# Kernel optimization log

Measured on AMD Instinct MI355X. Metric: run time of the kernel, lower is better.

The kernel has to match this reference:

```python
import jax, jax.numpy as jnp
import numpy as np

GRID = 10
C_IN = 4          # input_dim // (grid*grid) = 400 // 100
HID = 128         # lstm hidden_dim
NV = 6            # num_vehicles
PH = 10           # pred_horizon
BN_EPS = 1e-5


def setup_inputs() -> dict:
    key = jax.random.key(0)
    ks = jax.random.split(key, 20)
    def n(k, shape, scale=0.05):
        return jax.random.normal(k, shape, jnp.float32) * scale
    return {
        "observations": jax.random.normal(ks[0], (1024, 32, 400), jnp.float32),
        # CNN
        "conv1_w": n(ks[1], (16, C_IN, 3, 3)), "conv1_b": n(ks[2], (16,)),
        "conv2_w": n(ks[3], (32, 16, 3, 3)), "conv2_b": n(ks[4], (32,)),
        # FCN (BatchNorm in eval mode: running stats + affine)
        "fc1_w": n(ks[5], (128, 128)), "fc1_b": n(ks[6], (128,)),
        "bn1_gamma": jnp.ones((128,), jnp.float32), "bn1_beta": jnp.zeros((128,), jnp.float32),
        "bn1_mean": jnp.zeros((128,), jnp.float32), "bn1_var": jnp.ones((128,), jnp.float32),
        "fc2_w": n(ks[7], (64, 128)), "fc2_b": n(ks[8], (64,)),
        "bn2_gamma": jnp.ones((64,), jnp.float32), "bn2_beta": jnp.zeros((64,), jnp.float32),
        "bn2_mean": jnp.zeros((64,), jnp.float32), "bn2_var": jnp.ones((64,), jnp.float32),
        # encoder LSTM (torch gate order i,f,g,o; b = b_ih + b_hh fused)
        "enc_w_ih": n(ks[9], (4 * HID, 64)), "enc_w_hh": n(ks[10], (4 * HID, HID)),
        "enc_b": n(ks[11], (4 * HID,)),
        # decoder LSTM
        "dec_w_ih": n(ks[12], (4 * HID, HID)), "dec_w_hh": n(ks[13], (4 * HID, HID)),
        "dec_b": n(ks[14], (4 * HID,)),
        # output head
        "out_w": n(ks[15], (2 * NV, HID)), "out_b": n(ks[16], (2 * NV,)),
    }


def _conv(x, w, b):
    y = jax.lax.conv_general_dilated(x, w, (1, 1), "SAME",
                                     dimension_numbers=("NCHW", "OIHW", "NCHW"))
    return y + b[None, :, None, None]


def _maxpool2(x):
    # MaxPool2d(2,2) with floor (drops odd trailing row/col) == VALID
    return jax.lax.reduce_window(x, -jnp.inf, jax.lax.max, (1, 1, 2, 2), (1, 1, 2, 2), "VALID")


def _bn(x, g, b, m, v):
    return (x - m) * jax.lax.rsqrt(v + BN_EPS) * g + b


def _lstm_cell(x, h, c, w_ih, w_hh, b):
    gates = x @ w_ih.T + h @ w_hh.T + b
    i, f, g, o = jnp.split(gates, 4, axis=-1)
    c_new = jax.nn.sigmoid(f) * c + jax.nn.sigmoid(i) * jnp.tanh(g)
    h_new = jax.nn.sigmoid(o) * jnp.tanh(c_new)
    return h_new, c_new


def reference(observations, conv1_w, conv1_b, conv2_w, conv2_b,
              fc1_w, fc1_b, bn1_gamma, bn1_beta, bn1_mean, bn1_var,
              fc2_w, fc2_b, bn2_gamma, bn2_beta, bn2_mean, bn2_var,
              enc_w_ih, enc_w_hh, enc_b, dec_w_ih, dec_w_hh, dec_b,
              out_w, out_b):
    B, T, D = observations.shape
    # ---- fuse the per-frame Python loop: batch all B*T frames at once ----
    x = observations.reshape(B * T, C_IN, GRID, GRID)
    x = _maxpool2(jax.nn.relu(_conv(x, conv1_w, conv1_b)))   # [BT,16,5,5]
    x = _maxpool2(jax.nn.relu(_conv(x, conv2_w, conv2_b)))   # [BT,32,2,2]
    x = x.reshape(B * T, -1)                                 # [BT,128]
    x = jax.nn.relu(_bn(x @ fc1_w.T + fc1_b, bn1_gamma, bn1_beta, bn1_mean, bn1_var))
    x = jax.nn.relu(_bn(x @ fc2_w.T + fc2_b, bn2_gamma, bn2_beta, bn2_mean, bn2_var))
    feats = x.reshape(B, T, 64)

    # ---- encoder LSTM ----
    h0 = jnp.zeros((B, HID), feats.dtype)
    c0 = jnp.zeros((B, HID), feats.dtype)
    def enc_step(carry, xt):
        h, c = carry
        h, c = _lstm_cell(xt, h, c, enc_w_ih, enc_w_hh, enc_b)
        return (h, c), h
    (h_n, c_n), hs = jax.lax.scan(enc_step, (h0, c0), jnp.swapaxes(feats, 0, 1))
    dec_x = hs[-1]  # encoder_output[:, -1]

    def dec_step(carry, _):
        x_in, h, c = carry
        h, c = _lstm_cell(x_in, h, c, dec_w_ih, dec_w_hh, dec_b)
        pred = h @ out_w.T + out_b
        return (h, h, c), pred
    _, preds = jax.lax.scan(dec_step, (dec_x, h_n, c_n), None, length=PH)
    return jnp.swapaxes(preds, 0, 1)  # [B, PH, 2*NV]
```

## Files before the change

kernel.cpp:

```cpp
#include <hip/hip_runtime.h>
#include <hip/hip_bf16.h>
#include <hip/hip_fp16.h>

constexpr int GT = 32768;
constexpr int TSEQ = 32;

typedef _Float16 h2 __attribute__((ext_vector_type(2)));

#if defined(__has_builtin)
#if __has_builtin(__builtin_amdgcn_fdot2)
#define FDOT2(a, b, c) __builtin_amdgcn_fdot2((a), (b), (c), false)
#endif
#endif
#ifndef FDOT2
#define FDOT2(a, b, c) fmaf((float)(a).x, (float)(b).x, fmaf((float)(a).y, (float)(b).y, (c)))
#endif

__device__ __forceinline__ h2 pack2(float a, float b) {
  h2 v; v.x = (_Float16)a; v.y = (_Float16)b; return v;
}

constexpr size_t OBS_T  = 0;
constexpr size_t POOL1H = 13107200;
constexpr size_t POOL2H = 0;
constexpr size_t Y1H    = 2097152;
constexpr size_t FEATSH = 19660800;
constexpr size_t GX     = 0;
constexpr size_t WB     = 26214400;
constexpr size_t W_C1   = WB + 0;
constexpr size_t W_C2H  = WB + 576;
constexpr size_t W_F1H  = WB + 2880;
constexpr size_t B_F1   = WB + 11072;
constexpr size_t W_F2H  = WB + 11200;
constexpr size_t B_F2   = WB + 15296;
constexpr size_t W_ENCXH= WB + 15360;
constexpr size_t W_ENCHH= WB + 31744;
constexpr size_t B_ENC  = WB + 64512;
constexpr size_t W_DECH = WB + 65024;
constexpr size_t B_DEC  = WB + 97792;

__device__ __forceinline__ float sigf(float x)  { return 1.f / (1.f + __expf(-x)); }
__device__ __forceinline__ float tanhfast(float x) { return 1.f - 2.f / (__expf(2.f * x) + 1.f); }

__global__ __launch_bounds__(256) void k_setup(
    const float* __restrict__ c1w, const float* __restrict__ c2w,
    const float* __restrict__ f1w, const float* __restrict__ f1b,
    const float* __restrict__ g1, const float* __restrict__ be1,
    const float* __restrict__ m1, const float* __restrict__ v1,
    const float* __restrict__ f2w, const float* __restrict__ f2b,
    const float* __restrict__ g2, const float* __restrict__ be2,
    const float* __restrict__ m2, const float* __restrict__ v2,
    const float* __restrict__ ewih, const float* __restrict__ ewhh, const float* __restrict__ eb,
    const float* __restrict__ dwih, const float* __restrict__ dwhh, const float* __restrict__ db,
    float* __restrict__ ws) {
  h2* wsh = (h2*)ws;
  long i = (long)blockIdx.x * 256 + threadIdx.x;
  if (i < 576)  { int c = i & 15, r = i >> 4; ws[W_C1 + i] = c1w[c * 36 + r]; return; }
  i -= 576;
  if (i < 2304) { int co = i & 31, q = i >> 5; int ci2 = q / 9, t9 = q % 9;
    wsh[W_C2H + i] = pack2(c2w[co * 144 + (2 * ci2) * 9 + t9],
                           c2w[co * 144 + (2 * ci2 + 1) * 9 + t9]); return; }
  i -= 2304;
  if (i < 8192) { int j = i & 127, q = i >> 7; int co2 = q >> 2, pos = q & 3;
    float s = g1[j] * rsqrtf(v1[j] + 1e-5f);
    wsh[W_F1H + i] = pack2(f1w[j * 128 + 8 * co2 + pos] * s,
                           f1w[j * 128 + 8 * co2 + 4 + pos] * s); return; }
  i -= 8192;
  if (i < 128) { int j = i; float s = g1[j] * rsqrtf(v1[j] + 1e-5f);
    ws[B_F1 + i] = (f1b[j] - m1[j]) * s + be1[j]; return; }
  i -= 128;
  if (i < 4096) { int j = i & 63, k2 = i >> 6;
    float s = g2[j] * rsqrtf(v2[j] + 1e-5f);
    wsh[W_F2H + i] = pack2(f2w[j * 128 + 2 * k2] * s,
                           f2w[j * 128 + 2 * k2 + 1] * s); return; }
  i -= 4096;
  if (i < 64) { int j = i; float s = g2[j] * rsqrtf(v2[j] + 1e-5f);
    ws[B_F2 + i] = (f2b[j] - m2[j]) * s + be2[j]; return; }
  i -= 64;
  if (i < 16384) { int r = i & 511, k2 = i >> 9;
    int u = r >> 2, gt = r & 3, jr = gt * 128 + u;
    wsh[W_ENCXH + i] = pack2(ewih[jr * 64 + 2 * k2], ewih[jr * 64 + 2 * k2 + 1]); return; }
  i -= 16384;
  if (i < 32768) { int r = i & 511, k2 = i >> 9;
    int u = r >> 2, gt = r & 3, jr = gt * 128 + u;
    wsh[W_ENCHH + i] = pack2(ewhh[jr * 128 + 2 * k2], ewhh[jr * 128 + 2 * k2 + 1]); return; }
  i -= 32768;
  if (i < 512) { int u = i >> 2, gt = i & 3; ws[B_ENC + i] = eb[gt * 128 + u]; return; }
  i -= 512;
  if (i < 32768) { int r = i & 511, k2 = i >> 9;
    int u = r >> 2, gt = r & 3, jr = gt * 128 + u;
    wsh[W_DECH + i] = pack2(dwih[jr * 128 + 2 * k2] + dwhh[jr * 128 + 2 * k2],
                            dwih[jr * 128 + 2 * k2 + 1] + dwhh[jr * 128 + 2 * k2 + 1]); return; }
  i -= 32768;
  if (i < 512) { int u = i >> 2, gt = i & 3; ws[B_DEC + i] = db[gt * 128 + u]; return; }
}

__global__ __launch_bounds__(256) void k_transpose(const float* __restrict__ obs,
                                                   float* __restrict__ obsT) {
  __shared__ float tile[64][65];
  int tp0 = blockIdx.x * 64;
  int b0  = blockIdx.y * 64;
  int q     = threadIdx.x & 15;
  int rbase = threadIdx.x >> 4;
  #pragma unroll
  for (int rr = 0; rr < 4; ++rr) {
    int row = rbase + rr * 16;
    const float4 v = *(const float4*)(obs + (size_t)(b0 + row) * 12800 + tp0 + q * 4);
    tile[row][q * 4 + 0] = v.x;
    tile[row][q * 4 + 1] = v.y;
    tile[row][q * 4 + 2] = v.z;
    tile[row][q * 4 + 3] = v.w;
  }
  __syncthreads();
  int lane = threadIdx.x & 63;
  int grp  = threadIdx.x >> 6;
  for (int cc = 0; cc < 16; ++cc) {
    int col = grp * 16 + cc;
    int tp = tp0 + col;
    int t = tp / 400, p = tp % 400;
    obsT[(size_t)p * GT + t * 1024 + b0 + lane] = tile[lane][col];
  }
}

__global__ __launch_bounds__(256) void k_conv1(const float* __restrict__ obsT,
                                               const float* __restrict__ wT,
                                               const float* __restrict__ bias,
                                               h2* __restrict__ pool1h) {
  int g = blockIdx.x * 256 + threadIdx.x;
  int pos = blockIdx.y;
  int py = pos / 5, px = pos % 5;
  float acc[4][16];
  #pragma unroll
  for (int s = 0; s < 4; ++s)
    #pragma unroll
    for (int c = 0; c < 16; ++c) acc[s][c] = 0.f;

  #pragma unroll 1
  for (int ci = 0; ci < 4; ++ci) {
    float p[16];
    #pragma unroll
    for (int r = 0; r < 4; ++r) {
      int iy = 2 * py + r - 1;
      #pragma unroll
      for (int cx = 0; cx < 4; ++cx) {
        int ix = 2 * px + cx - 1;
        bool ok = ((unsigned)iy < 10u) && ((unsigned)ix < 10u);
        p[r * 4 + cx] = ok ? obsT[(size_t)(ci * 100 + iy * 10 + ix) * GT + g] : 0.f;
      }
    }
    #pragma unroll
    for (int t9 = 0; t9 < 9; ++t9) {
      int ky = t9 / 3, kx = t9 % 3;
      const float* w = wT + ((ci * 9 + t9) << 4);
      float wv[16];
      #pragma unroll
      for (int c = 0; c < 16; ++c) wv[c] = w[c];
      #pragma unroll
      for (int dy = 0; dy < 2; ++dy)
        #pragma unroll
        for (int dx = 0; dx < 2; ++dx) {
          float xv = p[(dy + ky) * 4 + (dx + kx)];
          #pragma unroll
          for (int c = 0; c < 16; ++c)
            acc[dy * 2 + dx][c] = fmaf(wv[c], xv, acc[dy * 2 + dx][c]);
        }
    }
  }
  float m[16];
  #pragma unroll
  for (int c = 0; c < 16; ++c) {
    float v = fmaxf(fmaxf(acc[0][c], acc[1][c]), fmaxf(acc[2][c], acc[3][c]));
    m[c] = fmaxf(v + bias[c], 0.f);
  }
  #pragma unroll
  for (int c2 = 0; c2 < 8; ++c2)
    pool1h[(size_t)(c2 * 25 + pos) * GT + g] = pack2(m[2 * c2], m[2 * c2 + 1]);
}

__global__ __launch_bounds__(256) void k_conv2h(const h2* __restrict__ pool1h,
                                                const h2* __restrict__ wch,
                                                const float* __restrict__ bias,
                                                h2* __restrict__ pool2h) {
  int g = blockIdx.x * 256 + threadIdx.x;
  int pos = blockIdx.y & 3;
  int h = blockIdx.y >> 2;
  int py = pos >> 1, px = pos & 1;
  float acc[4][8];
  #pragma unroll
  for (int s = 0; s < 4; ++s)
    #pragma unroll
    for (int c = 0; c < 8; ++c) acc[s][c] = 0.f;
  const h2 hz = pack2(0.f, 0.f);

  #pragma unroll 1
  for (int ci2 = 0; ci2 < 8; ++ci2) {
    h2 p[16];
    #pragma unroll
    for (int r = 0; r < 4; ++r) {
      int iy = 2 * py + r - 1;
      #pragma unroll
      for (int cx = 0; cx < 4; ++cx) {
        int ix = 2 * px + cx - 1;
        bool ok = ((unsigned)iy < 5u) && ((unsigned)ix < 5u);
        p[r * 4 + cx] = ok ? pool1h[(size_t)(ci2 * 25 + iy * 5 + ix) * GT + g] : hz;
      }
    }
    #pragma unroll
    for (int t9 = 0; t9 < 9; ++t9) {
      int ky = t9 / 3, kx = t9 % 3;
      const h2* w = wch + (ci2 * 9 + t9) * 32 + h * 8;
      h2 wv[8];
      #pragma unroll
      for (int c = 0; c < 8; ++c) wv[c] = w[c];
      #pragma unroll
      for (int dy = 0; dy < 2; ++dy)
        #pragma unroll
        for (int dx = 0; dx < 2; ++dx) {
          h2 xv = p[(dy + ky) * 4 + (dx + kx)];
          #pragma unroll
          for (int c = 0; c < 8; ++c)
            acc[dy * 2 + dx][c] = FDOT2(xv, wv[c], acc[dy * 2 + dx][c]);
        }
    }
  }
  float m[8];
  #pragma unroll
  for (int c = 0; c < 8; ++c) {
    float v = fmaxf(fmaxf(acc[0][c], acc[1][c]), fmaxf(acc[2][c], acc[3][c]));
    m[c] = fmaxf(v + bias[h * 8 + c], 0.f);
  }
  #pragma unroll
  for (int c2 = 0; c2 < 4; ++c2) {
    int q = (h * 4 + c2) * 4 + pos;
    pool2h[(size_t)q * GT + g] = pack2(m[2 * c2], m[2 * c2 + 1]);
  }
}

__global__ __launch_bounds__(256) void k_fc16h(const h2* __restrict__ x,
                                               const h2* __restrict__ WT,
                                               const float* __restrict__ bf,
                                               h2* __restrict__ y, int K2, int J) {
  int g = blockIdx.x * 256 + threadIdx.x;
  int j0 = blockIdx.y * 16;
  float acc[16];
  #pragma unroll
  for (int c = 0; c < 16; ++c) acc[c] = 0.f;
  for (int k2 = 0; k2 < K2; ++k2) {
    h2 xv = x[(size_t)k2 * GT + g];
    const h2* w = WT + (size_t)k2 * J + j0;
    #pragma unroll
    for (int c = 0; c < 16; ++c) acc[c] = FDOT2(xv, w[c], acc[c]);
  }
  #pragma unroll
  for (int c2 = 0; c2 < 8; ++c2) {
    float a = fmaxf(acc[2 * c2] + bf[j0 + 2 * c2], 0.f);
    float b = fmaxf(acc[2 * c2 + 1] + bf[j0 + 2 * c2 + 1], 0.f);
    y[(size_t)(j0 / 2 + c2) * GT + g] = pack2(a, b);
  }
}

__global__ __launch_bounds__(256) void k_xgatesh(const h2* __restrict__ featsh,
                                                 const h2* __restrict__ wxh,
                                                 const float* __restrict__ br,
                                                 float* __restrict__ gx) {
  int t  = blockIdx.x >> 2;
  int bq = blockIdx.x & 3;
  int b  = bq * 256 + threadIdx.x;
  int r0 = blockIdx.y * 32;
  float acc[32];
  #pragma unroll
  for (int i = 0; i < 32; ++i) acc[i] = br[r0 + i];
  const h2* xcol = featsh + (size_t)t * 1024 + b;
  for (int k2 = 0; k2 < 32; ++k2) {
    h2 xv = xcol[(size_t)k2 * GT];
    const h2* w = wxh + k2 * 512 + r0;
    #pragma unroll
    for (int i = 0; i < 32; ++i) acc[i] = FDOT2(xv, w[i], acc[i]);
  }
  float* gxs = gx + (size_t)t * 524288 + (size_t)b * 512 + r0;
  #pragma unroll
  for (int i = 0; i < 32; ++i) gxs[i] = acc[i];
}

__global__ __launch_bounds__(512, 2) void k_seq8(
    const float* __restrict__ gx,
    const h2* __restrict__ WENCH, const h2* __restrict__ WDECH,
    const float* __restrict__ bdec,
    const float* __restrict__ ow, const float* __restrict__ ob,
    float* __restrict__ out) {
  const int tid = threadIdx.x;
  const int bl  = tid & 3;
  const int kg  = (tid >> 2) & 1;
  const int g   = tid >> 3;
  const int r0  = g * 8;
  const int bown = blockIdx.x * 4 + bl;

  __shared__ h2 wA[16384];
  __shared__ h2 wB[16384];
  __shared__ h2 hbufh[2][4 * 68];
  __shared__ h2 owl2[12 * 68];

  for (int i = tid; i < 2 * 4 * 68; i += 512) ((h2*)hbufh)[i] = pack2(0.f, 0.f);
  for (int i = tid; i < 768; i += 512) {
    int o = i >> 6, k2 = i & 63;
    owl2[o * 68 + k2] = pack2(ow[o * 128 + 2 * k2], ow[o * 128 + 2 * k2 + 1]);
  }
  const float obv = (tid < 48) ? ob[tid >> 2] : 0.f;

  for (int c = tid; c < 4096; c += 512) {
    int p = c >> 7, kgc = (c >> 6) & 1, gc = c & 63;
    const uint4* gp = (const uint4*)(WENCH + (size_t)(kgc * 32 + p) * 512 + gc * 8);
    *(uint4*)&wA[(size_t)c * 4] = gp[0];
    *(uint4*)&wB[(size_t)c * 4] = gp[1];
  }

  float c0 = 0.f, c1 = 0.f;
  const h2* wAp = &wA[(kg * 64 + g) * 4];
  const h2* wBp = &wB[(kg * 64 + g) * 4];
  __syncthreads();

  int cur = 0;

  for (int t = 0; t < TSEQ; ++t) {
    const float* gb0 = gx + (size_t)t * 524288 + (size_t)bown * 512 + r0;
    const float4 ga = *(const float4*)gb0;
    const float4 gb = *(const float4*)(gb0 + 4);

    float acc[8];
    #pragma unroll
    for (int r = 0; r < 8; ++r) acc[r] = 0.f;

    const h2* hp = &hbufh[cur][bl * 68 + kg * 32];
    #pragma unroll
    for (int pc = 0; pc < 8; ++pc) {
      h2 hh[4];
      *(uint4*)hh = *(const uint4*)&hp[pc * 4];
      #pragma unroll
      for (int j = 0; j < 4; ++j) {
        const int p = pc * 4 + j;
        h2 wa[4], wb[4];
        *(uint4*)wa = *(const uint4*)&wAp[p * 512];
        *(uint4*)wb = *(const uint4*)&wBp[p * 512];
        acc[0] = FDOT2(hh[j], wa[0], acc[0]);
        acc[1] = FDOT2(hh[j], wa[1], acc[1]);
        acc[2] = FDOT2(hh[j], wa[2], acc[2]);
        acc[3] = FDOT2(hh[j], wa[3], acc[3]);
        acc[4] = FDOT2(hh[j], wb[0], acc[4]);
        acc[5] = FDOT2(hh[j], wb[1], acc[5]);
        acc[6] = FDOT2(hh[j], wb[2], acc[6]);
        acc[7] = FDOT2(hh[j], wb[3], acc[7]);
      }
    }
    float D[8];
    #pragma unroll
    for (int r = 0; r < 8; ++r) D[r] = acc[r] + __shfl_xor(acc[r], 4, 64);

    const float gi0 = D[0] + ga.x, gf0 = D[1] + ga.y, gg0 = D[2] + ga.z, go0 = D[3] + ga.w;
    const float gi1 = D[4] + gb.x, gf1 = D[5] + gb.y, gg1 = D[6] + gb.z, go1 = D[7] + gb.w;
    c0 = sigf(gf0) * c0 + sigf(gi0) * tanhfast(gg0);
    c1 = sigf(gf1) * c1 + sigf(gi1) * tanhfast(gg1);
    const float hn0 = sigf(go0) * tanhfast(c0);
    const float hn1 = sigf(go1) * tanhfast(c1);
    if (kg == 0) hbufh[cur ^ 1][bl * 68 + g] = pack2(hn0, hn1);
    __syncthreads();
    cur ^= 1;
  }

  for (int c = tid; c < 4096; c += 512) {
    int p = c >> 7, kgc = (c >> 6) & 1, gc = c & 63;
    const uint4* gp = (const uint4*)(WDECH + (size_t)(kgc * 32 + p) * 512 + gc * 8);
    *(uint4*)&wA[(size_t)c * 4] = gp[0];
    *(uint4*)&wB[(size_t)c * 4] = gp[1];
  }
  const float4 bda = *(const float4*)(bdec + r0);
  const float4 bdb = *(const float4*)(bdec + r0 + 4);
  __syncthreads();

  for (int t = 0; t < 10; ++t) {
    float acc[8];
    #pragma unroll
    for (int r = 0; r < 8; ++r) acc[r] = 0.f;

    const h2* hp = &hbufh[cur][bl * 68 + kg * 32];
    #pragma unroll
    for (int pc = 0; pc < 8; ++pc) {
      h2 hh[4];
      *(uint4*)hh = *(const uint4*)&hp[pc * 4];
      #pragma unroll
      for (int j = 0; j < 4; ++j) {
        const int p = pc * 4 + j;
        h2 wa[4], wb[4];
        *(uint4*)wa = *(const uint4*)&wAp[p * 512];
        *(uint4*)wb = *(const uint4*)&wBp[p * 512];
        acc[0] = FDOT2(hh[j], wa[0], acc[0]);
        acc[1] = FDOT2(hh[j], wa[1], acc[1]);
        acc[2] = FDOT2(hh[j], wa[2], acc[2]);
        acc[3] = FDOT2(hh[j], wa[3], acc[3]);
        acc[4] = FDOT2(hh[j], wb[0], acc[4]);
        acc[5] = FDOT2(hh[j], wb[1], acc[5]);
        acc[6] = FDOT2(hh[j], wb[2], acc[6]);
        acc[7] = FDOT2(hh[j], wb[3], acc[7]);
      }
    }
    float D[8];
    #pragma unroll
    for (int r = 0; r < 8; ++r) D[r] = acc[r] + __shfl_xor(acc[r], 4, 64);

    const float gi0 = D[0] + bda.x, gf0 = D[1] + bda.y, gg0 = D[2] + bda.z, go0 = D[3] + bda.w;
    const float gi1 = D[4] + bdb.x, gf1 = D[5] + bdb.y, gg1 = D[6] + bdb.z, go1 = D[7] + bdb.w;
    c0 = sigf(gf0) * c0 + sigf(gi0) * tanhfast(gg0);
    c1 = sigf(gf1) * c1 + sigf(gi1) * tanhfast(gg1);
    const float hn0 = sigf(go0) * tanhfast(c0);
    const float hn1 = sigf(go1) * tanhfast(c1);
    if (kg == 0) hbufh[cur ^ 1][bl * 68 + g] = pack2(hn0, hn1);
    __syncthreads();
    cur ^= 1;
    if (tid < 48) {
      const int o  = tid >> 2;
      const int bh = tid & 3;
      const h2* hh = &hbufh[cur][bh * 68];
      const h2* wo = &owl2[o * 68];
      float oacc = obv;
      #pragma unroll
      for (int k2 = 0; k2 < 64; ++k2) oacc = FDOT2(hh[k2], wo[k2], oacc);
      out[(blockIdx.x * 4 + bh) * 120 + t * 12 + o] = oacc;
    }
  }
}

extern "C" void kernel_launch(void* const* d_in, const int* in_sizes, int n_in,
                              void* d_out, int out_size, void* d_ws, size_t ws_size,
                              hipStream_t stream) {
  const float* obs  = (const float*)d_in[0];
  const float* c1w  = (const float*)d_in[1];
  const float* c1b  = (const float*)d_in[2];
  const float* c2w  = (const float*)d_in[3];
  const float* c2b  = (const float*)d_in[4];
  const float* f1w  = (const float*)d_in[5];
  const float* f1b  = (const float*)d_in[6];
  const float* g1   = (const float*)d_in[7];
  const float* be1  = (const float*)d_in[8];
  const float* m1   = (const float*)d_in[9];
  const float* v1   = (const float*)d_in[10];
  const float* f2w  = (const float*)d_in[11];
  const float* f2b  = (const float*)d_in[12];
  const float* g2   = (const float*)d_in[13];
  const float* be2  = (const float*)d_in[14];
  const float* m2   = (const float*)d_in[15];
  const float* v2   = (const float*)d_in[16];
  const float* ewih = (const float*)d_in[17];
  const float* ewhh = (const float*)d_in[18];
  const float* eb   = (const float*)d_in[19];
  const float* dwih = (const float*)d_in[20];
  const float* dwhh = (const float*)d_in[21];
  const float* db   = (const float*)d_in[22];
  const float* ow   = (const float*)d_in[23];
  const float* ob   = (const float*)d_in[24];
  float* ws  = (float*)d_ws;
  h2*    wsh = (h2*)d_ws;
  float* out = (float*)d_out;

  k_setup<<<384, 256, 0, stream>>>(c1w, c2w, f1w, f1b, g1, be1, m1, v1,
                                   f2w, f2b, g2, be2, m2, v2,
                                   ewih, ewhh, eb, dwih, dwhh, db, ws);
  k_transpose<<<dim3(200, 16), 256, 0, stream>>>(obs, ws + OBS_T);
  k_conv1<<<dim3(128, 25), 256, 0, stream>>>(ws + OBS_T, ws + W_C1, c1b, wsh + POOL1H);
  k_conv2h<<<dim3(128, 16), 256, 0, stream>>>(wsh + POOL1H, wsh + W_C2H, c2b, wsh + POOL2H);
  k_fc16h<<<dim3(128, 8), 256, 0, stream>>>(wsh + POOL2H, wsh + W_F1H, ws + B_F1,
                                            wsh + Y1H, 64, 128);
  k_fc16h<<<dim3(128, 4), 256, 0, stream>>>(wsh + Y1H, wsh + W_F2H, ws + B_F2,
                                            wsh + FEATSH, 64, 64);
  k_xgatesh<<<dim3(128, 16), 256, 0, stream>>>(wsh + FEATSH, wsh + W_ENCXH, ws + B_ENC,
                                               ws + GX);
  k_seq8<<<256, 512, 0, stream>>>(ws + GX, wsh + W_ENCHH, wsh + W_DECH,
                                  ws + B_DEC, ow, ob, out);
}
```

Before: 390.7 us.

## Keep LSTM recurrent weights in registers instead of shared memory

```diff
diff --git a/kernel.cpp b/kernel.cpp
--- a/kernel.cpp
+++ b/kernel.cpp
@@ -289,14 +289,11 @@
     const float* __restrict__ ow, const float* __restrict__ ob,
     float* __restrict__ out) {
   const int tid = threadIdx.x;
-  const int bl  = tid & 3;
-  const int kg  = (tid >> 2) & 1;
-  const int g   = tid >> 3;
-  const int r0  = g * 8;
-  const int bown = blockIdx.x * 4 + bl;
-
-  __shared__ h2 wA[16384];
-  __shared__ h2 wB[16384];
+  const int bl2 = tid & 1;
+  const int kg  = (tid >> 1) & 1;
+  const int g   = tid >> 2;
+  const int b0  = blockIdx.x * 4 + bl2 * 2;
+
   __shared__ h2 hbufh[2][4 * 68];
   __shared__ h2 owl2[12 * 68];
 
@@ -307,53 +304,43 @@
   }
   const float obv = (tid < 48) ? ob[tid >> 2] : 0.f;
 
-  for (int c = tid; c < 4096; c += 512) {
-    int p = c >> 7, kgc = (c >> 6) & 1, gc = c & 63;
-    const uint4* gp = (const uint4*)(WENCH + (size_t)(kgc * 32 + p) * 512 + gc * 8);
-    *(uint4*)&wA[(size_t)c * 4] = gp[0];
-    *(uint4*)&wB[(size_t)c * 4] = gp[1];
-  }
+  h2 wreg[32][4];
+  #pragma unroll
+  for (int p = 0; p < 32; ++p)
+    *(uint4*)wreg[p] = *(const uint4*)(WENCH + (size_t)(kg * 32 + p) * 512 + g * 4);
 
   float c0 = 0.f, c1 = 0.f;
-  const h2* wAp = &wA[(kg * 64 + g) * 4];
-  const h2* wBp = &wB[(kg * 64 + g) * 4];
   __syncthreads();
-
   int cur = 0;
 
   for (int t = 0; t < TSEQ; ++t) {
-    const float* gb0 = gx + (size_t)t * 524288 + (size_t)bown * 512 + r0;
-    const float4 ga = *(const float4*)gb0;
-    const float4 gb = *(const float4*)(gb0 + 4);
+    const float4 ga = *(const float4*)(gx + (size_t)t * 524288 + (size_t)b0 * 512 + g * 4);
+    const float4 gb = *(const float4*)(gx + (size_t)t * 524288 + (size_t)(b0 + 1) * 512 + g * 4);
 
     float acc[8];
     #pragma unroll
     for (int r = 0; r < 8; ++r) acc[r] = 0.f;
 
-    const h2* hp = &hbufh[cur][bl * 68 + kg * 32];
-    #pragma unroll
-    for (int pc = 0; pc < 8; ++pc) {
-      h2 hh[4];
-      *(uint4*)hh = *(const uint4*)&hp[pc * 4];
-      #pragma unroll
-      for (int j = 0; j < 4; ++j) {
-        const int p = pc * 4 + j;
-        h2 wa[4], wb[4];
-        *(uint4*)wa = *(const uint4*)&wAp[p * 512];
-        *(uint4*)wb = *(const uint4*)&wBp[p * 512];
-        acc[0] = FDOT2(hh[j], wa[0], acc[0]);
-        acc[1] = FDOT2(hh[j], wa[1], acc[1]);
-        acc[2] = FDOT2(hh[j], wa[2], acc[2]);
-        acc[3] = FDOT2(hh[j], wa[3], acc[3]);
-        acc[4] = FDOT2(hh[j], wb[0], acc[4]);
-        acc[5] = FDOT2(hh[j], wb[1], acc[5]);
-        acc[6] = FDOT2(hh[j], wb[2], acc[6]);
-        acc[7] = FDOT2(hh[j], wb[3], acc[7]);
+    #pragma unroll
+    for (int b = 0; b < 2; ++b) {
+      const h2* hp = &hbufh[cur][(bl2 * 2 + b) * 68 + kg * 32];
+      #pragma unroll
+      for (int pc = 0; pc < 8; ++pc) {
+        h2 hh[4];
+        *(uint4*)hh = *(const uint4*)&hp[pc * 4];
+        #pragma unroll
+        for (int j = 0; j < 4; ++j) {
+          const int p = pc * 4 + j;
+          acc[b * 4 + 0] = FDOT2(hh[j], wreg[p][0], acc[b * 4 + 0]);
+          acc[b * 4 + 1] = FDOT2(hh[j], wreg[p][1], acc[b * 4 + 1]);
+          acc[b * 4 + 2] = FDOT2(hh[j], wreg[p][2], acc[b * 4 + 2]);
+          acc[b * 4 + 3] = FDOT2(hh[j], wreg[p][3], acc[b * 4 + 3]);
+        }
       }
     }
     float D[8];
     #pragma unroll
-    for (int r = 0; r < 8; ++r) D[r] = acc[r] + __shfl_xor(acc[r], 4, 64);
+    for (int r = 0; r < 8; ++r) D[r] = acc[r] + __shfl_xor(acc[r], 2, 64);
 
     const float gi0 = D[0] + ga.x, gf0 = D[1] + ga.y, gg0 = D[2] + ga.z, go0 = D[3] + ga.w;
     const float gi1 = D[4] + gb.x, gf1 = D[5] + gb.y, gg1 = D[6] + gb.z, go1 = D[7] + gb.w;
@@ -361,58 +348,57 @@
     c1 = sigf(gf1) * c1 + sigf(gi1) * tanhfast(gg1);
     const float hn0 = sigf(go0) * tanhfast(c0);
     const float hn1 = sigf(go1) * tanhfast(c1);
-    if (kg == 0) hbufh[cur ^ 1][bl * 68 + g] = pack2(hn0, hn1);
+    if (kg == 0) {
+      _Float16* hf = (_Float16*)&hbufh[cur ^ 1][0];
+      hf[(bl2 * 2 + 0) * 136 + g] = (_Float16)hn0;
+      hf[(bl2 * 2 + 1) * 136 + g] = (_Float16)hn1;
+    }
     __syncthreads();
     cur ^= 1;
   }
 
-  for (int c = tid; c < 4096; c += 512) {
-    int p = c >> 7, kgc = (c >> 6) & 1, gc = c & 63;
-    const uint4* gp = (const uint4*)(WDECH + (size_t)(kgc * 32 + p) * 512 + gc * 8);
-    *(uint4*)&wA[(size_t)c * 4] = gp[0];
-    *(uint4*)&wB[(size_t)c * 4] = gp[1];
-  }
-  const float4 bda = *(const float4*)(bdec + r0);
-  const float4 bdb = *(const float4*)(bdec + r0 + 4);
-  __syncthreads();
+  #pragma unroll
+  for (int p = 0; p < 32; ++p)
+    *(uint4*)wreg[p] = *(const uint4*)(WDECH + (size_t)(kg * 32 + p) * 512 + g * 4);
+  const float4 bd = *(const float4*)(bdec + g * 4);
 
   for (int t = 0; t < 10; ++t) {
     float acc[8];
     #pragma unroll
     for (int r = 0; r < 8; ++r) acc[r] = 0.f;
 
-    const h2* hp = &hbufh[cur][bl * 68 + kg * 32];
-    #pragma unroll
-    for (int pc = 0; pc < 8; ++pc) {
-      h2 hh[4];
-      *(uint4*)hh = *(const uint4*)&hp[pc * 4];
-      #pragma unroll
-      for (int j = 0; j < 4; ++j) {
-        const int p = pc * 4 + j;
-        h2 wa[4], wb[4];
-        *(uint4*)wa = *(const uint4*)&wAp[p * 512];
-        *(uint4*)wb = *(const uint4*)&wBp[p * 512];
-        acc[0] = FDOT2(hh[j], wa[0], acc[0]);
-        acc[1] = FDOT2(hh[j], wa[1], acc[1]);
-        acc[2] = FDOT2(hh[j], wa[2], acc[2]);
-        acc[3] = FDOT2(hh[j], wa[3], acc[3]);
-        acc[4] = FDOT2(hh[j], wb[0], acc[4]);
-        acc[5] = FDOT2(hh[j], wb[1], acc[5]);
-        acc[6] = FDOT2(hh[j], wb[2], acc[6]);
-        acc[7] = FDOT2(hh[j], wb[3], acc[7]);
+    #pragma unroll
+    for (int b = 0; b < 2; ++b) {
+      const h2* hp = &hbufh[cur][(bl2 * 2 + b) * 68 + kg * 32];
+      #pragma unroll
+      for (int pc = 0; pc < 8; ++pc) {
+        h2 hh[4];
+        *(uint4*)hh = *(const uint4*)&hp[pc * 4];
+        #pragma unroll
+        for (int j = 0; j < 4; ++j) {
+          const int p = pc * 4 + j;
+          acc[b * 4 + 0] = FDOT2(hh[j], wreg[p][0], acc[b * 4 + 0]);
+          acc[b * 4 + 1] = FDOT2(hh[j], wreg[p][1], acc[b * 4 + 1]);
+          acc[b * 4 + 2] = FDOT2(hh[j], wreg[p][2], acc[b * 4 + 2]);
+          acc[b * 4 + 3] = FDOT2(hh[j], wreg[p][3], acc[b * 4 + 3]);
+        }
       }
     }
     float D[8];
     #pragma unroll
-    for (int r = 0; r < 8; ++r) D[r] = acc[r] + __shfl_xor(acc[r], 4, 64);
-
-    const float gi0 = D[0] + bda.x, gf0 = D[1] + bda.y, gg0 = D[2] + bda.z, go0 = D[3] + bda.w;
-    const float gi1 = D[4] + bdb.x, gf1 = D[5] + bdb.y, gg1 = D[6] + bdb.z, go1 = D[7] + bdb.w;
+    for (int r = 0; r < 8; ++r) D[r] = acc[r] + __shfl_xor(acc[r], 2, 64);
+
+    const float gi0 = D[0] + bd.x, gf0 = D[1] + bd.y, gg0 = D[2] + bd.z, go0 = D[3] + bd.w;
+    const float gi1 = D[4] + bd.x, gf1 = D[5] + bd.y, gg1 = D[6] + bd.z, go1 = D[7] + bd.w;
     c0 = sigf(gf0) * c0 + sigf(gi0) * tanhfast(gg0);
     c1 = sigf(gf1) * c1 + sigf(gi1) * tanhfast(gg1);
     const float hn0 = sigf(go0) * tanhfast(c0);
     const float hn1 = sigf(go1) * tanhfast(c1);
-    if (kg == 0) hbufh[cur ^ 1][bl * 68 + g] = pack2(hn0, hn1);
+    if (kg == 0) {
+      _Float16* hf = (_Float16*)&hbufh[cur ^ 1][0];
+      hf[(bl2 * 2 + 0) * 136 + g] = (_Float16)hn0;
+      hf[(bl2 * 2 + 1) * 136 + g] = (_Float16)hn1;
+    }
     __syncthreads();
     cur ^= 1;
     if (tid < 48) {
```

Measured after the change: 381.9 us. -2.3%, faster.
